# Optimization experiments

Hardware: AMD Instinct MI355X
Metric: run time of the kernel (lower is better)

## Reference

```python
import jax, jax.numpy as jnp
import numpy as np

EMBED_DIM = 1024
BATCH = 4
SEQ = 2048


def setup_inputs() -> dict:
    key = jax.random.key(0)
    ks = jax.random.split(key, 9)
    D = EMBED_DIM
    s = 1.0 / np.sqrt(D)
    inputs = jax.random.normal(ks[0], (BATCH, SEQ, D), dtype=jnp.float32)
    rotation_params = jax.random.normal(ks[1], (D, D), dtype=jnp.float32) * s
    entangle_params = jax.random.normal(ks[2], (D, D), dtype=jnp.float32) * s
    Wq = jax.random.normal(ks[3], (D, D), dtype=jnp.float32) * s
    bq = jax.random.normal(ks[4], (D,), dtype=jnp.float32) * 0.01
    Wk = jax.random.normal(ks[5], (D, D), dtype=jnp.float32) * s
    bk = jax.random.normal(ks[6], (D,), dtype=jnp.float32) * 0.01
    Wv = jax.random.normal(ks[7], (D, D), dtype=jnp.float32) * s
    bv = jax.random.normal(ks[8], (D,), dtype=jnp.float32) * 0.01
    # causal mask: True = masked out (matches torch masked_fill semantics)
    mask = jnp.triu(jnp.ones((SEQ, SEQ), dtype=bool), k=1)
    return {"inputs": inputs, "rotation_params": rotation_params,
            "entangle_params": entangle_params, "Wq": Wq, "bq": bq,
            "Wk": Wk, "bk": bk, "Wv": Wv, "bv": bv, "mask": mask}


def reference(inputs, rotation_params, entangle_params, Wq, bq, Wk, bk, Wv, bv, mask):
    D = inputs.shape[-1]
    # q = Linear(x) @ R^T ; k = Linear(x) @ E^T ; v = Linear(x)
    q = (jnp.einsum('bsd,ed->bse', inputs, Wq) + bq) @ rotation_params.T
    k = (jnp.einsum('bsd,ed->bse', inputs, Wk) + bk) @ entangle_params.T
    v = jnp.einsum('bsd,ed->bse', inputs, Wv) + bv
    scores = jnp.einsum('bqd,bkd->bqk', q, k) / jnp.sqrt(jnp.float32(D))
    scores = jnp.where(mask, jnp.float32(-jnp.inf), scores)
    probs = jax.nn.softmax(scores, axis=-1)  # dropout=0.0 -> identity
    return jnp.einsum('bqk,bkd->bqd', probs, v)
```

## Files before the change

### kernel.cpp

```cpp
#include <hip/hip_runtime.h>
#include <hip/hip_bf16.h>
#include <stdint.h>
#include <math.h>

#define DD 1024
#define SS 2048
#define BB 4

typedef __bf16 bf16;
typedef __bf16 bf16x8 __attribute__((ext_vector_type(8)));
typedef __bf16 bf16x4 __attribute__((ext_vector_type(4)));
typedef float f32x4 __attribute__((ext_vector_type(4)));

__device__ __forceinline__ void gload_lds16(const bf16* g, bf16* l) {
  __builtin_amdgcn_global_load_lds(
      (const __attribute__((address_space(1))) void*)g,
      (__attribute__((address_space(3))) void*)l, 16, 0, 0);
}

__global__ __launch_bounds__(256) void prep_all(
    const float* __restrict__ x, const float* __restrict__ R,
    const float* __restrict__ E, const float* __restrict__ Wv,
    const float* __restrict__ Wq, const float* __restrict__ Wk,
    const float* __restrict__ bq, const float* __restrict__ bk,
    const float* __restrict__ bv, bf16* __restrict__ xb,
    bf16* __restrict__ Rb, bf16* __restrict__ Eb, bf16* __restrict__ Wvb,
    bf16* __restrict__ WqT, bf16* __restrict__ WkT, float* __restrict__ bias,
    float* __restrict__ rowsums) {
  int bid = blockIdx.x;
  int t = threadIdx.x;
  if (bid < 11264) {
    const float* src;
    bf16* dst;
    int base;
    if (bid < 8192) { src = x; dst = xb; base = bid; }
    else if (bid < 9216) { src = R; dst = Rb; base = bid - 8192; }
    else if (bid < 10240) { src = E; dst = Eb; base = bid - 9216; }
    else { src = Wv; dst = Wvb; base = bid - 10240; }
    int i = (base * 256 + t) * 4;
    float4 v = *(const float4*)(src + i);
    bf16x4 o;
    o.x = (bf16)v.x; o.y = (bf16)v.y; o.z = (bf16)v.z; o.w = (bf16)v.w;
    *(bf16x4*)(dst + i) = o;
  } else if (bid < 13312) {
    int r2 = bid - 11264;
    const float* src = (r2 >= 1024) ? Wk : Wq;
    bf16* dst = (r2 >= 1024) ? WkT : WqT;
    int rem = r2 & 1023;
    int bx = rem & 31, by = rem >> 5;
    __shared__ float tile[32][33];
    int tx = t & 31, ty = t >> 5;
    int xcol = bx * 32 + tx;
    int y0 = by * 32;
    for (int r = ty; r < 32; r += 8)
      tile[r][tx] = src[(y0 + r) * DD + xcol];
    __syncthreads();
    int dx = by * 32 + tx;
    int dy0 = bx * 32;
    for (int r = ty; r < 32; r += 8)
      dst[(dy0 + r) * DD + dx] = (bf16)tile[tx][r];
  } else if (bid < 16384) {
    int e = bid - 13312;
    if (e >= 2048) { if (t == 0) bias[e] = bv[e - 2048]; return; }
    const float* M = (e < 1024) ? R : E;
    const float* bb = (e < 1024) ? bq : bk;
    int row = e & 1023;
    float s = 0.f;
    for (int f = t; f < DD; f += 256) s += M[row * DD + f] * bb[f];
    for (int o = 32; o >= 1; o >>= 1) s += __shfl_xor(s, o, 64);
    __shared__ float red[4];
    if ((t & 63) == 0) red[t >> 6] = s;
    __syncthreads();
    if (t == 0) bias[e] = red[0] + red[1] + red[2] + red[3];
  } else {
    int idx = (bid - 16384) * 256 + t;
    rowsums[idx] = 0.f;
  }
}

template <int MODE>
__global__ __launch_bounds__(256, 4)
void gemm_bt(const bf16* __restrict__ Ag, long lda, long sAb,
             const bf16* __restrict__ Bg, long ldb, long sBb,
             void* __restrict__ Cg, long ldc, long sCb,
             const float* __restrict__ bias, float scale, int K,
             bf16* __restrict__ vTp, float* __restrict__ rowsums) {
  __shared__ __align__(16) bf16 smem[16384];
  bf16* As = smem;
  bf16* Bs = smem + 8192;

  int bx = blockIdx.x, by = blockIdx.y, bz = blockIdx.z;
  if (MODE == 0 || MODE == 1) {
    int nx = (int)gridDim.x;
    int nwg = nx * (int)gridDim.y;
    int id = by * nx + bx;
    int xcd = id & 7, rest = id >> 3;
    int q8 = nwg >> 3, r8 = nwg & 7;
    int wg = (xcd < r8 ? xcd * (q8 + 1) : r8 * (q8 + 1) + (xcd - r8) * q8)
             + rest;
    bx = wg % nx;
    by = wg / nx;
  }
  if (MODE == 1) {
    int q = bx;
    by = (int)((sqrtf(8.f * q + 1.f) - 1.f) * 0.5f);
    while ((by + 1) * (by + 2) / 2 <= q) by++;
    while (by * (by + 1) / 2 > q) by--;
    bx = q - by * (by + 1) / 2;
  }
  if (MODE == 2) by = 15 - by;
  long m0 = (long)by * 128, n0 = (long)bx * 128;
  const bf16* A = Ag + (long)bz * sAb + m0 * lda;
  const bf16* Bp = Bg + (long)bz * sBb + n0 * ldb;

  int t = threadIdx.x;
  int w = t >> 6, l = t & 63;
  int lr = l >> 2;
  int lc = (((l & 3) ^ (lr & 3)) * 8);
  int quad = l >> 4, ln = l & 15;
  int wm = w >> 1, wn = w & 1;
  int rdoff = ((quad ^ (ln & 3)) * 8);

  int Keff = (MODE == 2) ? (by + 1) * 128 : K;

  f32x4 acc[4][4];
#pragma unroll
  for (int i = 0; i < 4; i++)
#pragma unroll
    for (int j = 0; j < 4; j++) acc[i][j] = f32x4{0.f, 0.f, 0.f, 0.f};

  const bf16* a_base = As + (wm * 64 + ln) * 32 + rdoff;
  const bf16* b_base = Bs + (wn * 64 + ln) * 32 + rdoff;
  long arow0 = (long)(w * 16 + lr);

#define STG(p, kc0)                                                         \
  {                                                                         \
    int kc = (kc0) + lc;                                                    \
    gload_lds16(A + arow0 * lda + kc, As + (p) * 4096 + w * 512);           \
    gload_lds16(A + (arow0 + 64) * lda + kc,                                \
                As + (p) * 4096 + 2048 + w * 512);                          \
    gload_lds16(Bp + arow0 * ldb + kc, Bs + (p) * 4096 + w * 512);          \
    gload_lds16(Bp + (arow0 + 64) * ldb + kc,                               \
                Bs + (p) * 4096 + 2048 + w * 512);                          \
  }

  STG(0, 0);
  int cur = 0;
  for (int k = 0; k < Keff; k += 32) {
    asm volatile("s_waitcnt vmcnt(0)" ::: "memory");
    __builtin_amdgcn_s_barrier();
    __builtin_amdgcn_sched_barrier(0);
    if (k + 32 < Keff) STG(cur ^ 1, k + 32);
    bf16x8 af[4], bfr[4];
#pragma unroll
    for (int i = 0; i < 4; i++) {
      af[i] = *(const bf16x8*)(a_base + cur * 4096 + i * 512);
      bfr[i] = *(const bf16x8*)(b_base + cur * 4096 + i * 512);
    }
#pragma unroll
    for (int i = 0; i < 4; i++)
#pragma unroll
      for (int j = 0; j < 4; j++)
        acc[i][j] = __builtin_amdgcn_mfma_f32_16x16x32_bf16(
            af[i], bfr[j], acc[i][j], 0, 0, 0);
    cur ^= 1;
  }
#undef STG
  __syncthreads();

  if (MODE == 0) {
    if (vTp && n0 >= 2048) {
      int d0 = (int)n0 - 2048;
      int b = (int)(m0 >> 11);
      int s0 = (int)(m0 & 2047);
#pragma unroll
      for (int i = 0; i < 4; i++) {
        int sb = wm * 64 + i * 16 + quad * 4;
#pragma unroll
        for (int j = 0; j < 4; j++) {
          int d = wn * 64 + j * 16 + ln;
          float bv_ = bias[n0 + d];
#pragma unroll
          for (int r = 0; r < 4; r++)
            smem[d * 128 + ((sb + r) ^ (ln << 3))] = (bf16)(acc[i][j][r] + bv_);
        }
      }
      __syncthreads();
      int d = t >> 1, h = t & 1;
      bf16* dst = vTp + (long)b * DD * SS + (long)(d0 + d) * SS + s0 + h * 64;
#pragma unroll
      for (int j = 0; j < 8; j++) {
        int sbase = h * 64 + j * 8;
        bf16x8 v = *(const bf16x8*)(smem + d * 128 + (sbase ^ ((d & 15) << 3)));
        *(bf16x8*)(dst + j * 8) = v;
      }
    } else {
      bf16* C = (bf16*)Cg + (long)bz * sCb + m0 * ldc + n0;
#pragma unroll
      for (int i = 0; i < 4; i++) {
        int rb = wm * 64 + i * 16 + quad * 4;
#pragma unroll
        for (int j = 0; j < 4; j++) {
          int col = wn * 64 + j * 16 + ln;
          float bv_ = bias ? bias[n0 + col] : 0.f;
#pragma unroll
          for (int r = 0; r < 4; r++)
            C[(long)(rb + r) * ldc + col] = (bf16)(acc[i][j][r] + bv_);
        }
      }
    }
  } else if (MODE == 1) {
#pragma unroll
    for (int i = 0; i < 4; i++) {
      int rb = wm * 64 + i * 16 + quad * 4;
#pragma unroll
      for (int j = 0; j < 4; j++) {
        int col = wn * 64 + j * 16 + ln;
#pragma unroll
        for (int r = 0; r < 4; r++) {
          int row = rb + r;
          float p = 0.f;
          if (n0 + col <= m0 + row) p = __expf(acc[i][j][r] * scale);
          smem[row * 128 + (col ^ ((row & 15) << 3))] = (bf16)p;
        }
      }
    }
    __syncthreads();
    int row = t >> 1, h = t & 1;
    bf16* P = (bf16*)Cg + (long)bz * sCb + (m0 + row) * ldc + n0;
    float rsum = 0.f;
#pragma unroll
    for (int jj = 0; jj < 8; jj++) {
      int p8 = h * 8 + jj;
      int slot = p8 ^ (row & 15);
      bf16x8 v = *(const bf16x8*)(smem + row * 128 + slot * 8);
#pragma unroll
      for (int e = 0; e < 8; e++) rsum += (float)v[e];
      *(bf16x8*)(P + p8 * 8) = v;
    }
    atomicAdd(&rowsums[(long)bz * SS + m0 + row], rsum);
  } else {
    float* C = (float*)Cg + (long)bz * sCb + m0 * ldc + n0;
    const float* rs = rowsums + (long)bz * SS + m0;
#pragma unroll
    for (int i = 0; i < 4; i++) {
      int rb = wm * 64 + i * 16 + quad * 4;
      float inv[4];
#pragma unroll
      for (int r = 0; r < 4; r++) inv[r] = 1.f / rs[rb + r];
#pragma unroll
      for (int j = 0; j < 4; j++) {
        int col = wn * 64 + j * 16 + ln;
#pragma unroll
        for (int r = 0; r < 4; r++)
          C[(long)(rb + r) * ldc + col] = acc[i][j][r] * inv[r];
      }
    }
  }
}

extern "C" void kernel_launch(void* const* d_in, const int* in_sizes, int n_in,
                              void* d_out, int out_size, void* d_ws,
                              size_t ws_size, hipStream_t stream) {
  const float* x = (const float*)d_in[0];
  const float* R = (const float*)d_in[1];
  const float* E = (const float*)d_in[2];
  const float* Wq = (const float*)d_in[3];
  const float* bq = (const float*)d_in[4];
  const float* Wk = (const float*)d_in[5];
  const float* bk = (const float*)d_in[6];
  const float* Wv = (const float*)d_in[7];
  const float* bv = (const float*)d_in[8];
  float* out = (float*)d_out;

  char* ws = (char*)d_ws;
  bf16* qkv = (bf16*)ws;
  bf16* vT = (bf16*)(ws + 50331648);
  bf16* probs = (bf16*)(ws + 67108864);
  float* rowsums = (float*)(ws + 100663296);
  char* sr = ws + 101711872;
  bf16* xb = (bf16*)sr;
  bf16* Rb = (bf16*)(sr + 16777216);
  bf16* Eb = Rb + 1024 * 1024;
  bf16* WqT = (bf16*)(sr + 20971520);
  bf16* WkT = WqT + 1024 * 1024;
  bf16* wcat = (bf16*)(sr + 25165824);
  float* bias = (float*)(sr + 31457280);

  prep_all<<<16416, 256, 0, stream>>>(x, R, E, Wv, Wq, Wk, bq, bk, bv, xb, Rb,
                                      Eb, wcat + 2048 * DD, WqT, WkT, bias,
                                      rowsums);

  gemm_bt<0><<<dim3(8, 8, 2), 256, 0, stream>>>(
      Rb, DD, 1024 * 1024, WqT, DD, 1024 * 1024, wcat, DD, 1024 * 1024,
      nullptr, 1.f, DD, nullptr, nullptr);

  gemm_bt<0><<<dim3(24, 64, 1), 256, 0, stream>>>(xb, DD, 0, wcat, DD, 0, qkv,
                                                  3072, 0, bias, 1.f, DD, vT,
                                                  nullptr);

  gemm_bt<1><<<dim3(136, 1, BB), 256, 0, stream>>>(
      qkv, 3072, (long)SS * 3072, qkv + 1024, 3072, (long)SS * 3072, probs,
      SS, (long)SS * SS, nullptr, 0.03125f, DD, nullptr, rowsums);

  gemm_bt<2><<<dim3(8, 16, BB), 256, 0, stream>>>(
      probs, SS, (long)SS * SS, vT, SS, (long)DD * SS, out,
      DD, (long)SS * DD, nullptr, 1.f, SS, nullptr, rowsums);
}
```

Before: 298.1 us.

## Add 256x256-tile 8-wave QKV projection GEMM with phased LDS pipeline

Replaces the 128x128-tile generic GEMM for the fused QKV projection with a dedicated 512-thread kernel computing 256x256 output tiles. It uses a hand-scheduled four-phase double-buffered global-to-LDS pipeline with explicit waitcnt, barriers and setprio around the MFMA blocks. The larger tile raises arithmetic intensity and cuts redundant global loads. The V-transpose epilogue is moved into this kernel in two halves through LDS, and the generic GEMM loses its transpose path. The cost is higher register and LDS pressure, with only two workgroups per CU and fewer total workgroups, which may hurt occupancy.

```diff
diff --git a/kernel.cpp b/kernel.cpp
--- a/kernel.cpp
+++ b/kernel.cpp
@@ -78,6 +78,141 @@
   }
 }
 
+#define STGA(p, h, kt)                                                       \
+  gload_lds16(A + (long)((h) * 128 + w * 16 + srow) * DD + (kt) * 32 + scg,  \
+              As + (p) * 8192 + (h) * 4096 + w * 512)
+#define STGB(p, h, kt)                                                       \
+  gload_lds16(B + (long)((h) * 128 + w * 16 + srow) * DD + (kt) * 32 + scg,  \
+              Bs + (p) * 8192 + (h) * 4096 + w * 512)
+
+#define PHASE(p, q, WAITN, ...)                                              \
+  {                                                                          \
+    bf16x8 af[4];                                                            \
+    _Pragma("unroll") for (int i_ = 0; i_ < 4; i_++)                         \
+        af[i_] = *(const bf16x8*)(a_base + (p) * 8192 + (q) * 2048 +         \
+                                  i_ * 512);                                 \
+    if ((q) == 0) {                                                          \
+      _Pragma("unroll") for (int j_ = 0; j_ < 4; j_++)                       \
+          bfr[j_] = *(const bf16x8*)(b_base + (p) * 8192 + j_ * 512);        \
+    }                                                                        \
+    __VA_ARGS__;                                                             \
+    __builtin_amdgcn_s_barrier();                                            \
+    asm volatile("s_waitcnt lgkmcnt(0)" ::: "memory");                       \
+    __builtin_amdgcn_sched_barrier(0);                                       \
+    __builtin_amdgcn_s_setprio(1);                                           \
+    _Pragma("unroll") for (int i_ = 0; i_ < 4; i_++)                         \
+        _Pragma("unroll") for (int j_ = 0; j_ < 4; j_++) acc[(q)*4 + i_][j_] \
+        = __builtin_amdgcn_mfma_f32_16x16x32_bf16(af[i_], bfr[j_],           \
+                                                  acc[(q)*4 + i_][j_], 0, 0, \
+                                                  0);                        \
+    __builtin_amdgcn_s_setprio(0);                                           \
+    __builtin_amdgcn_sched_barrier(0);                                       \
+    if ((WAITN) == 2) asm volatile("s_waitcnt vmcnt(2)" ::: "memory");       \
+    if ((WAITN) == 0) asm volatile("s_waitcnt vmcnt(0)" ::: "memory");       \
+    __builtin_amdgcn_s_barrier();                                            \
+    __builtin_amdgcn_sched_barrier(0);                                       \
+  }
+
+__global__ __launch_bounds__(512, 2) void gemm256_qkv(
+    const bf16* __restrict__ Ag, const bf16* __restrict__ Bg,
+    bf16* __restrict__ Cg, const float* __restrict__ bias,
+    bf16* __restrict__ vTp) {
+  __shared__ __align__(16) bf16 smem[32768];
+  bf16* As = smem;
+  bf16* Bs = smem + 16384;
+
+  int id = (int)blockIdx.y * 12 + (int)blockIdx.x;
+  int wg = (id & 7) * 48 + (id >> 3);
+  int bx = wg % 12, by = wg / 12;
+  long m0 = (long)by * 256, n0 = (long)bx * 256;
+  const bf16* A = Ag + m0 * DD;
+  const bf16* B = Bg + n0 * DD;
+
+  int t = threadIdx.x;
+  int w = t >> 6, l = t & 63;
+  int wm = w >> 2, wn = w & 3;
+  int ln = l & 15, quad = l >> 4;
+
+  int srow = l >> 2;
+  int scg = ((l & 3) ^ ((l >> 3) & 3)) * 8;
+  int rdslot = (quad ^ ((ln >> 1) & 3)) * 8;
+  const bf16* a_base = As + (wm * 128 + ln) * 32 + rdslot;
+  const bf16* b_base = Bs + (wn * 64 + ln) * 32 + rdslot;
+
+  f32x4 acc[8][4];
+#pragma unroll
+  for (int i = 0; i < 8; i++)
+#pragma unroll
+    for (int j = 0; j < 4; j++) acc[i][j] = f32x4{0.f, 0.f, 0.f, 0.f};
+  bf16x8 bfr[4];
+
+  STGA(0, 0, 0); STGA(0, 1, 0);
+  STGB(0, 0, 0); STGB(0, 1, 0);
+  STGB(1, 0, 1); STGB(1, 1, 1);
+  asm volatile("s_waitcnt vmcnt(2)" ::: "memory");
+  __builtin_amdgcn_s_barrier();
+  __builtin_amdgcn_sched_barrier(0);
+
+#pragma unroll 1
+  for (int t2 = 0; t2 < 30; t2 += 2) {
+    PHASE(0, 0, -1, { STGA(1, 0, t2 + 1); STGA(1, 1, t2 + 1); })
+    PHASE(0, 1, 2, { STGB(0, 0, t2 + 2); STGB(0, 1, t2 + 2); })
+    PHASE(1, 0, -1, { STGA(0, 0, t2 + 2); STGA(0, 1, t2 + 2); })
+    PHASE(1, 1, 2, { STGB(1, 0, t2 + 3); STGB(1, 1, t2 + 3); })
+  }
+  PHASE(0, 0, -1, { STGA(1, 0, 31); STGA(1, 1, 31); })
+  PHASE(0, 1, 0, {})
+  PHASE(1, 0, -1, {})
+  PHASE(1, 1, -1, {})
+
+  if (n0 < 2048) {
+    bf16* C = Cg + m0 * 3072 + n0;
+#pragma unroll
+    for (int mf = 0; mf < 8; mf++) {
+      int rb = wm * 128 + mf * 16 + quad * 4;
+#pragma unroll
+      for (int nf = 0; nf < 4; nf++) {
+        int col = wn * 64 + nf * 16 + ln;
+        float bv_ = bias[n0 + col];
+#pragma unroll
+        for (int r = 0; r < 4; r++)
+          C[(long)(rb + r) * 3072 + col] = (bf16)(acc[mf][nf][r] + bv_);
+      }
+    }
+  } else {
+    int d0 = (int)n0 - 2048;
+    int b = (int)(m0 >> 11);
+    int s0 = (int)(m0 & 2047);
+    for (int h = 0; h < 2; ++h) {
+      __syncthreads();
+      if (wm == h) {
+#pragma unroll
+        for (int mf = 0; mf < 8; mf++) {
+          int sl = mf * 16 + quad * 4;
+#pragma unroll
+          for (int nf = 0; nf < 4; nf++) {
+            int d = wn * 64 + nf * 16 + ln;
+            float bv_ = bias[n0 + d];
+#pragma unroll
+            for (int r = 0; r < 4; r++)
+              smem[d * 128 + ((sl + r) ^ ((d & 7) << 3))] =
+                  (bf16)(acc[mf][nf][r] + bv_);
+          }
+        }
+      }
+      __syncthreads();
+      int d = t >> 1, sh = t & 1;
+      bf16* dst = vTp + (long)b * DD * SS + (long)(d0 + d) * SS + s0 +
+                  h * 128 + sh * 64;
+#pragma unroll
+      for (int c = 0; c < 8; ++c) {
+        int sc = (sh * 64 + c * 8) ^ ((d & 7) << 3);
+        *(bf16x8*)(dst + c * 8) = *(const bf16x8*)(smem + d * 128 + sc);
+      }
+    }
+  }
+}
+
 template <int MODE>
 __global__ __launch_bounds__(256, 4)
 void gemm_bt(const bf16* __restrict__ Ag, long lda, long sAb,
@@ -169,44 +304,17 @@
   __syncthreads();
 
   if (MODE == 0) {
-    if (vTp && n0 >= 2048) {
-      int d0 = (int)n0 - 2048;
-      int b = (int)(m0 >> 11);
-      int s0 = (int)(m0 & 2047);
-#pragma unroll
-      for (int i = 0; i < 4; i++) {
-        int sb = wm * 64 + i * 16 + quad * 4;
-#pragma unroll
-        for (int j = 0; j < 4; j++) {
-          int d = wn * 64 + j * 16 + ln;
-          float bv_ = bias[n0 + d];
-#pragma unroll
-          for (int r = 0; r < 4; r++)
-            smem[d * 128 + ((sb + r) ^ (ln << 3))] = (bf16)(acc[i][j][r] + bv_);
-        }
-      }
-      __syncthreads();
-      int d = t >> 1, h = t & 1;
-      bf16* dst = vTp + (long)b * DD * SS + (long)(d0 + d) * SS + s0 + h * 64;
-#pragma unroll
-      for (int j = 0; j < 8; j++) {
-        int sbase = h * 64 + j * 8;
-        bf16x8 v = *(const bf16x8*)(smem + d * 128 + (sbase ^ ((d & 15) << 3)));
-        *(bf16x8*)(dst + j * 8) = v;
-      }
-    } else {
-      bf16* C = (bf16*)Cg + (long)bz * sCb + m0 * ldc + n0;
-#pragma unroll
-      for (int i = 0; i < 4; i++) {
-        int rb = wm * 64 + i * 16 + quad * 4;
-#pragma unroll
-        for (int j = 0; j < 4; j++) {
-          int col = wn * 64 + j * 16 + ln;
-          float bv_ = bias ? bias[n0 + col] : 0.f;
-#pragma unroll
-          for (int r = 0; r < 4; r++)
-            C[(long)(rb + r) * ldc + col] = (bf16)(acc[i][j][r] + bv_);
-        }
+    bf16* C = (bf16*)Cg + (long)bz * sCb + m0 * ldc + n0;
+#pragma unroll
+    for (int i = 0; i < 4; i++) {
+      int rb = wm * 64 + i * 16 + quad * 4;
+#pragma unroll
+      for (int j = 0; j < 4; j++) {
+        int col = wn * 64 + j * 16 + ln;
+        float bv_ = bias ? bias[n0 + col] : 0.f;
+#pragma unroll
+        for (int r = 0; r < 4; r++)
+          C[(long)(rb + r) * ldc + col] = (bf16)(acc[i][j][r] + bv_);
       }
     }
   } else if (MODE == 1) {
@@ -295,9 +403,7 @@
       Rb, DD, 1024 * 1024, WqT, DD, 1024 * 1024, wcat, DD, 1024 * 1024,
       nullptr, 1.f, DD, nullptr, nullptr);
 
-  gemm_bt<0><<<dim3(24, 64, 1), 256, 0, stream>>>(xb, DD, 0, wcat, DD, 0, qkv,
-                                                  3072, 0, bias, 1.f, DD, vT,
-                                                  nullptr);
+  gemm256_qkv<<<dim3(12, 32, 1), 512, 0, stream>>>(xb, wcat, qkv, bias, vT);
 
   gemm_bt<1><<<dim3(136, 1, BB), 256, 0, stream>>>(
       qkv, 3072, (long)SS * 3072, qkv + 1024, 3072, (long)SS * 3072, probs,
```

Result: no change. 294.3 us (-1.3%).
